# Optimization experiments

Hardware: AMD Instinct MI355X
Metric: run time of the kernel (lower is better)

The kernel has to match this reference:

```python
import jax, jax.numpy as jnp
import numpy as np

B, R, H, IN, L = 8, 128, 256, 512, 3
NH, DH = 4, H // 4  # attention heads


def _layernorm(x, g, b, eps=1e-5):
    mu = jnp.mean(x, axis=-1, keepdims=True)
    var = jnp.mean(jnp.square(x - mu), axis=-1, keepdims=True)
    return (x - mu) * jax.lax.rsqrt(var + eps) * g + b


def setup_inputs() -> dict:
    key = jax.random.key(0)
    ks = iter(jax.random.split(key, 40))
    s = 0.02
    d = {}
    d['x'] = jax.random.normal(next(ks), (B, IN), jnp.float32)
    d['We'] = jax.random.normal(next(ks), (IN, H), jnp.float32) * s
    d['be'] = jnp.zeros((H,), jnp.float32)
    # per-graph-layer params, stacked along leading L axis
    d['msg_W1'] = jax.random.normal(next(ks), (L, 2 * H, H), jnp.float32) * s
    d['msg_b1'] = jnp.zeros((L, H), jnp.float32)
    d['msg_W2'] = jax.random.normal(next(ks), (L, H, H), jnp.float32) * s
    d['msg_b2'] = jnp.zeros((L, H), jnp.float32)
    d['upd_W1'] = jax.random.normal(next(ks), (L, 2 * H, H), jnp.float32) * s
    d['upd_b1'] = jnp.zeros((L, H), jnp.float32)
    d['upd_W2'] = jax.random.normal(next(ks), (L, H, H), jnp.float32) * s
    d['upd_b2'] = jnp.zeros((L, H), jnp.float32)
    d['ln_g'] = jnp.ones((L, H), jnp.float32)
    d['ln_b'] = jnp.zeros((L, H), jnp.float32)
    d['rule_adj'] = jax.random.normal(next(ks), (R, R), jnp.float32)
    # multihead attention (4 heads)
    d['Wq'] = jax.random.normal(next(ks), (H, H), jnp.float32) * s
    d['bq'] = jnp.zeros((H,), jnp.float32)
    d['Wk'] = jax.random.normal(next(ks), (H, H), jnp.float32) * s
    d['bk'] = jnp.zeros((H,), jnp.float32)
    d['Wv'] = jax.random.normal(next(ks), (H, H), jnp.float32) * s
    d['bv'] = jnp.zeros((H,), jnp.float32)
    d['Wo'] = jax.random.normal(next(ks), (H, H), jnp.float32) * s
    d['bo'] = jnp.zeros((H,), jnp.float32)
    # readout MLP -> num_rules logits
    d['ro_W1'] = jax.random.normal(next(ks), (H, H), jnp.float32) * s
    d['ro_b1'] = jnp.zeros((H,), jnp.float32)
    d['ro_W2'] = jax.random.normal(next(ks), (H, R), jnp.float32) * s
    d['ro_b2'] = jnp.zeros((R,), jnp.float32)
    return d


def reference(x, We, be, msg_W1, msg_b1, msg_W2, msg_b2,
              upd_W1, upd_b1, upd_W2, upd_b2, ln_g, ln_b, rule_adj,
              Wq, bq, Wk, bk, Wv, bv, Wo, bo,
              ro_W1, ro_b1, ro_W2, ro_b2):
    # node encoder, broadcast to all rule-graph nodes: [B,R,H]
    h0 = x @ We + be
    h = jnp.broadcast_to(h0[:, None, :], (B, R, H))
    # rule adjacency with self-edges excluded (loop used i != j)
    A = jax.nn.sigmoid(rule_adj) * (1.0 - jnp.eye(R, dtype=rule_adj.dtype))  # [R,R]
    for l in range(L):
        # message_net(cat(h_i, h_j)) = relu(h_i@W1a + h_j@W1b + b1)@W2 + b2
        W1a, W1b = msg_W1[l][:H], msg_W1[l][H:]
        a = h @ W1a   # [B,R,H] (receiver i part)
        bb = h @ W1b  # [B,R,H] (sender j part)
        pre = jax.nn.relu(a[:, :, None, :] + bb[:, None, :, :] + msg_b1[l])  # [B,R,R,H]
        m = pre @ msg_W2[l] + msg_b2[l]  # [B,R,R,H] message from j to i
        agg = jnp.einsum('bijh,ij->bih', m, A)  # weighted sum over senders j
        # update_net(cat(h, agg))
        Wu1a, Wu1b = upd_W1[l][:H], upd_W1[l][H:]
        u = jax.nn.relu(h @ Wu1a + agg @ Wu1b + upd_b1[l]) @ upd_W2[l] + upd_b2[l]
        h = _layernorm(h + u, ln_g[l], ln_b[l])
    # multihead self-attention over nodes
    q = (h @ Wq + bq).reshape(B, R, NH, DH)
    k = (h @ Wk + bk).reshape(B, R, NH, DH)
    v = (h @ Wv + bv).reshape(B, R, NH, DH)
    logits = jnp.einsum('bqhd,bkhd->bhqk', q, k) / jnp.sqrt(jnp.float32(DH))
    attn = jax.nn.softmax(logits, axis=-1)
    pooled = jnp.einsum('bhqk,bkhd->bqhd', attn, v).reshape(B, R, H) @ Wo + bo
    g = jnp.mean(pooled, axis=1)  # [B,H]
    rule_logits = jax.nn.relu(g @ ro_W1 + ro_b1) @ ro_W2 + ro_b2
    rule_probabilities = jax.nn.softmax(rule_logits, axis=-1)  # [B,R]
    return rule_probabilities
```

## Files before the change

kernel.cpp:

```cpp
#include <hip/hip_runtime.h>
#include <math.h>

constexpr int NB  = 8;
constexpr int NR  = 128;
constexpr int HID = 256;
constexpr int NIN = 512;
constexpr int DHD = 64;
constexpr size_t SZ = (size_t)NB * NR * HID;

struct KP {
    const float *x, *We, *be, *msg_W1, *msg_b1, *msg_W2, *msg_b2;
    const float *upd_W1, *upd_b1, *upd_W2, *upd_b2, *ln_g, *ln_b, *rule_adj;
    const float *Wq, *bq, *Wk, *bk, *Wv, *bv, *Wo, *bo, *ro_W1, *ro_b1, *ro_W2, *ro_b2;
    float* out;
    float *N0, *N1, *N2;
    float *aB, *bbB, *p1B;
    float *aA, *bbA, *p1A;
    float *W2u, *mb2u, *Aw, *rsum;
    float *mW1s;
    float *h0g;
    float *c0g, *c1g;
    float *gacc;
    float *scratch;
};

__device__ __forceinline__ void gemm_core(
    float (&As)[16][68], float (&Bs)[16][64], int m0, int n0,
    const float* __restrict__ A, const float* __restrict__ B,
    float (&acc)[4][4])
{
    int tid = threadIdx.x;
    int ty = tid >> 4, tx = tid & 15;
    int arow = tid >> 2, acol = (tid & 3) << 2;
    int brow = tid >> 4, bcol = (tid & 15) << 2;
    int m = m0 + arow;

    float4 av = *(const float4*)&A[(size_t)m * HID + acol];
    float4 bv = *(const float4*)&B[(size_t)brow * HID + n0 + bcol];

    for (int k0 = 0; k0 < HID; k0 += 16) {
        As[acol + 0][arow] = av.x;
        As[acol + 1][arow] = av.y;
        As[acol + 2][arow] = av.z;
        As[acol + 3][arow] = av.w;
        *(float4*)&Bs[brow][bcol] = bv;
        __syncthreads();
        if (k0 + 16 < HID) {
            av = *(const float4*)&A[(size_t)m * HID + k0 + 16 + acol];
            bv = *(const float4*)&B[(size_t)(k0 + 16 + brow) * HID + n0 + bcol];
        }
#pragma unroll
        for (int kk = 0; kk < 16; ++kk) {
            float4 af = *(const float4*)&As[kk][ty << 2];
            float4 bf = *(const float4*)&Bs[kk][tx << 2];
            float a_[4] = {af.x, af.y, af.z, af.w};
            float b_[4] = {bf.x, bf.y, bf.z, bf.w};
#pragma unroll
            for (int i = 0; i < 4; ++i)
#pragma unroll
                for (int j = 0; j < 4; ++j) acc[i][j] += a_[i] * b_[j];
        }
        __syncthreads();
    }
}

__device__ __forceinline__ void gemv256w(
    const float* xs, const float* __restrict__ W,
    const float* __restrict__ bias, int relu, float* ys, float* red)
{
    int tid = threadIdx.x;
    int w = tid >> 6, l = tid & 63;
    float4 acc = {0.f, 0.f, 0.f, 0.f};
    const float* Wp = W + (size_t)(w * 64) * HID + l * 4;
    const float* xp = xs + w * 64;
#pragma unroll 16
    for (int kk = 0; kk < 64; ++kk) {
        float xv = xp[kk];
        float4 wv = *(const float4*)(Wp + (size_t)kk * HID);
        acc.x += xv * wv.x; acc.y += xv * wv.y;
        acc.z += xv * wv.z; acc.w += xv * wv.w;
    }
    *(float4*)&red[w * 256 + l * 4] = acc;
    __syncthreads();
    float v = red[tid] + red[256 + tid] + red[512 + tid] + red[768 + tid];
    if (bias) v += bias[tid];
    if (relu) v = fmaxf(v, 0.0f);
    ys[tid] = v;
    __syncthreads();
}

__device__ __forceinline__ void rows4_q(
    const float (&rows)[4][HID], const float* __restrict__ W,
    int col, int q, float o[4])
{
    o[0] = o[1] = o[2] = o[3] = 0.f;
    int kb = q * 64;
#pragma unroll 4
    for (int k0 = 0; k0 < 64; k0 += 4) {
        int k = kb + k0;
        float w0 = W[(size_t)(k + 0) * HID + col];
        float w1 = W[(size_t)(k + 1) * HID + col];
        float w2 = W[(size_t)(k + 2) * HID + col];
        float w3 = W[(size_t)(k + 3) * HID + col];
#pragma unroll
        for (int ii = 0; ii < 4; ++ii) {
            float4 rv = *(const float4*)&rows[ii][k];
            o[ii] += rv.x * w0 + rv.y * w1 + rv.z * w2 + rv.w * w3;
        }
    }
}

__device__ __forceinline__ void ln_stats4_q(
    float (&sred)[4][4][2], float (&mi)[4][2], const float v[4], int q)
{
    if (q == 0) {
        int w = threadIdx.x >> 6, l = threadIdx.x & 63;
        float s[4], qq[4];
#pragma unroll
        for (int ii = 0; ii < 4; ++ii) { s[ii] = v[ii]; qq[ii] = v[ii] * v[ii]; }
#pragma unroll
        for (int off = 32; off; off >>= 1) {
#pragma unroll
            for (int ii = 0; ii < 4; ++ii) {
                s[ii] += __shfl_xor(s[ii], off);
                qq[ii] += __shfl_xor(qq[ii], off);
            }
        }
        if (l == 0) {
#pragma unroll
            for (int ii = 0; ii < 4; ++ii) { sred[w][ii][0] = s[ii]; sred[w][ii][1] = qq[ii]; }
        }
    }
    __syncthreads();
    if (threadIdx.x < 4) {
        int r = threadIdx.x;
        float ss = sred[0][r][0] + sred[1][r][0] + sred[2][r][0] + sred[3][r][0];
        float qq = sred[0][r][1] + sred[1][r][1] + sred[2][r][1] + sred[3][r][1];
        float mu = ss * (1.0f / HID);
        mi[r][0] = mu;
        mi[r][1] = rsqrtf(qq * (1.0f / HID) - mu * mu + 1e-5f);
    }
    __syncthreads();
}

__global__ __launch_bounds__(256) void setup0_kernel(KP P) {
    __shared__ union {
        struct { float As[16][68]; float Bs[16][64]; } g;
        struct { float xs[NIN]; float part[8][32]; } e;
    } L;
    int blk = blockIdx.x;
    int t = threadIdx.x;

    if (blk < 32) {
        int rr = blk * 4 + (t >> 6);
        int l = t & 63;
        float s_loc = 0.f;
#pragma unroll
        for (int rep = 0; rep < 2; ++rep) {
            int j = l + rep * 64;
            float xv = P.rule_adj[rr * NR + j];
            float sg = 1.0f / (1.0f + expf(-xv));
            if (j == rr) sg = 0.0f;
            P.Aw[rr * NR + j] = sg;
            s_loc += sg;
        }
#pragma unroll
        for (int off = 32; off; off >>= 1) s_loc += __shfl_xor(s_loc, off);
        if (l == 0) P.rsum[rr] = s_loc;
    } else if (blk < 80) {
        int idx = blk - 32, l2 = idx >> 4, t16 = idx & 15;
        int m0 = (t16 >> 2) * 64, n0 = (t16 & 3) * 64;
        float acc[4][4] = {};
        gemm_core(L.g.As, L.g.Bs, m0, n0,
                  P.msg_W2 + (size_t)l2 * HID * HID,
                  P.upd_W1 + (size_t)l2 * 2 * HID * HID + (size_t)HID * HID,
                  acc);
        int ty = t >> 4, tx = t & 15;
        float* C = P.W2u + (size_t)l2 * HID * HID;
#pragma unroll
        for (int i = 0; i < 4; ++i) {
            int m = m0 + (ty << 2) + i, n = n0 + (tx << 2);
            float4 o = {acc[i][0], acc[i][1], acc[i][2], acc[i][3]};
            *(float4*)&C[(size_t)m * HID + n] = o;
        }
    } else if (blk < 83) {
        int l2 = blk - 80;
        const float* b2v = P.msg_b2 + l2 * HID;
        const float* Bm = P.upd_W1 + (size_t)l2 * 2 * HID * HID + (size_t)HID * HID;
        float acc = 0.f;
#pragma unroll 4
        for (int k = 0; k < HID; ++k) acc += b2v[k] * Bm[(size_t)k * HID + t];
        P.mb2u[l2 * HID + t] = acc;
    } else if (blk < 147) {
        int idx = blk - 83;
        int b = idx >> 3, s = idx & 7;
        L.e.xs[t]       = P.x[b * NIN + t];
        L.e.xs[256 + t] = P.x[b * NIN + 256 + t];
        __syncthreads();
        int c = t & 31, seg = t >> 5;
        int col = s * 32 + c;
        const float* Wp = P.We + (size_t)(seg * 64) * HID + col;
        const float* xp = L.e.xs + seg * 64;
        float acc = 0.f;
#pragma unroll 16
        for (int k = 0; k < 64; ++k) acc += xp[k] * Wp[(size_t)k * HID];
        L.e.part[seg][c] = acc;
        __syncthreads();
        if (t < 32) {
            float v = 0.f;
#pragma unroll
            for (int sg = 0; sg < 8; ++sg) v += L.e.part[sg][t];
            int cc = s * 32 + t;
            P.h0g[b * HID + cc] = v + P.be[cc];
        }
    } else if (blk < 163) {
        int base = (blk - 147) * 4096;
        for (int i = t; i < 4096; i += 256) {
            int o = base + i;
            P.mW1s[o] = P.msg_W1[o] + P.msg_W1[65536 + o];
        }
    } else {
        int pfid = blk - 163, npf = 256 - 163;
        const float* arr[11] = {P.We, P.msg_W1, P.msg_W2, P.upd_W1, P.upd_W2,
                                P.Wq, P.Wk, P.Wv, P.Wo, P.ro_W1, P.ro_W2};
        const int n4[11] = {32768, 98304, 49152, 98304, 49152,
                            16384, 16384, 16384, 16384, 16384, 8192};
        float s = 0.f;
        for (int a = 0; a < 11; ++a) {
            const float4* p4 = (const float4*)arr[a];
            for (int i = pfid * 256 + t; i < n4[a]; i += npf * 256) {
                float4 v = p4[i];
                s += v.x + v.y + v.z + v.w;
            }
        }
        if (s == 1.0e37f) P.scratch[pfid] = s;
    }
}

__global__ __launch_bounds__(256) void setup1_kernel(KP P) {
    __shared__ float h0s[HID], c0s[HID], p0s[HID], c1s[HID];
    __shared__ float red[1024];
    int b = blockIdx.x;
    int t = threadIdx.x;
    h0s[t] = P.h0g[b * HID + t];
    __syncthreads();
    gemv256w(h0s, P.upd_W1, nullptr, 0, c0s, red);
    gemv256w(h0s, P.mW1s, P.msg_b1, 1, p0s, red);
    gemv256w(p0s, P.W2u, P.mb2u, 0, c1s, red);
    P.c0g[b * HID + t] = c0s[t];
    P.c1g[b * HID + t] = c1s[t];
}

__global__ __launch_bounds__(1024) void layer0p_kernel(KP P) {
    __shared__ float h0s[HID];
    __shared__ float u1s[4][HID];
    __shared__ float nrm[4][HID];
    __shared__ float part4[4][4][HID];
    __shared__ float sred[4][4][2];
    __shared__ float mi[4][2];
    int blk = blockIdx.x;
    int m0 = blk * 4;
    int b = m0 >> 7, i0 = m0 & 127;
    int t = threadIdx.x;
    int col = t & 255, q = t >> 8;

    if (q == 0) {
        float h0v = P.h0g[b * HID + col];
        h0s[col] = h0v;
        float c0 = P.c0g[b * HID + col];
        float c1 = P.c1g[b * HID + col];
        float ubv = P.upd_b1[col];
#pragma unroll
        for (int ii = 0; ii < 4; ++ii)
            u1s[ii][col] = fmaxf(c0 + P.rsum[i0 + ii] * c1 + ubv, 0.0f);
    }
    __syncthreads();

    float o[4];
    rows4_q(u1s, P.upd_W2, col, q, o);
#pragma unroll
    for (int ii = 0; ii < 4; ++ii) part4[q][ii][col] = o[ii];
    __syncthreads();
    float v[4] = {0.f, 0.f, 0.f, 0.f};
    if (q == 0) {
        float h0v = h0s[col] + P.upd_b2[col];
#pragma unroll
        for (int ii = 0; ii < 4; ++ii)
            v[ii] = part4[0][ii][col] + part4[1][ii][col] + part4[2][ii][col]
                  + part4[3][ii][col] + h0v;
    }
    ln_stats4_q(sred, mi, v, q);
    if (q == 0) {
        float gv = P.ln_g[col], btv = P.ln_b[col];
#pragma unroll
        for (int ii = 0; ii < 4; ++ii) {
            float nv = (v[ii] - mi[ii][0]) * mi[ii][1] * gv + btv;
            nrm[ii][col] = nv;
            P.N0[(size_t)(m0 + ii) * HID + col] = nv;
        }
    }
    __syncthreads();

    const float* mW1a1 = P.msg_W1 + (size_t)1 * 2 * HID * HID;
    const float* uW1a1 = P.upd_W1 + (size_t)1 * 2 * HID * HID;
    const float* pw[3] = {mW1a1, mW1a1 + (size_t)HID * HID, uW1a1};
    float* po[3] = {P.aB, P.bbB, P.p1B};
#pragma unroll
    for (int p = 0; p < 3; ++p) {
        rows4_q(nrm, pw[p], col, q, o);
#pragma unroll
        for (int ii = 0; ii < 4; ++ii) part4[q][ii][col] = o[ii];
        __syncthreads();
        if (q == 0) {
#pragma unroll
            for (int ii = 0; ii < 4; ++ii)
                po[p][(size_t)(m0 + ii) * HID + col] =
                    part4[0][ii][col] + part4[1][ii][col] +
                    part4[2][ii][col] + part4[3][ii][col];
        }
        __syncthreads();
    }
}

__global__ __launch_bounds__(1024) void aggproj_kernel(
    const float* __restrict__ a, const float* __restrict__ bbv,
    const float* __restrict__ mb1, const float* __restrict__ Aw,
    const float* __restrict__ rsumv,
    const float* __restrict__ P1, const float* __restrict__ W2u,
    const float* __restrict__ mb2u, const float* __restrict__ ub1,
    const float* __restrict__ uW2, const float* __restrict__ ub2,
    const float* __restrict__ Nprev, const float* __restrict__ lng,
    const float* __restrict__ lnb, float* __restrict__ Nout,
    const float* __restrict__ pw0, const float* __restrict__ pb0, float* __restrict__ o0,
    const float* __restrict__ pw1, const float* __restrict__ pb1, float* __restrict__ o1,
    const float* __restrict__ pw2, const float* __restrict__ pb2, float* __restrict__ o2,
    float* __restrict__ gzero)
{
    __shared__ float ap[4][HID];
    __shared__ float u1s[4][HID];
    __shared__ float nrm[4][HID];
    __shared__ float awr[4][NR];
    __shared__ float part4[4][4][HID];
    __shared__ float sred[4][4][2];
    __shared__ float mi[4][2];
    int blk = blockIdx.x;
    int b  = blk >> 5;
    int i0 = (blk & 31) * 4;
    int m0 = b * NR + i0;
    int t  = threadIdx.x;
    int col = t & 255, q = t >> 8;

    if (gzero && blk == 0 && q == 0) {
#pragma unroll
        for (int i = 0; i < 8; ++i) gzero[i * 256 + col] = 0.f;
    }

    if (t < 512) awr[t >> 7][t & 127] = Aw[(i0 + (t >> 7)) * NR + (t & 127)];

    float bias = mb1[col];
    float ai[4];
#pragma unroll
    for (int ii = 0; ii < 4; ++ii)
        ai[ii] = a[(size_t)(m0 + ii) * HID + col] + bias;
    __syncthreads();

    {
        float acc[4] = {0.f, 0.f, 0.f, 0.f};
        const float* bbb = &bbv[(size_t)b * NR * HID + col];
        int jb = q * 32;
#pragma unroll 4
        for (int j = 0; j < 32; ++j) {
            float bj = bbb[(size_t)(jb + j) * HID];
#pragma unroll
            for (int ii = 0; ii < 4; ++ii) {
                float pre = fmaxf(ai[ii] + bj, 0.0f);
                acc[ii] += awr[ii][jb + j] * pre;
            }
        }
#pragma unroll
        for (int ii = 0; ii < 4; ++ii) part4[q][ii][col] = acc[ii];
        __syncthreads();
        if (q == 0) {
#pragma unroll
            for (int ii = 0; ii < 4; ++ii)
                ap[ii][col] = part4[0][ii][col] + part4[1][ii][col]
                            + part4[2][ii][col] + part4[3][ii][col];
        }
        __syncthreads();
    }

    {
        float o[4];
        rows4_q(ap, W2u, col, q, o);
#pragma unroll
        for (int ii = 0; ii < 4; ++ii) part4[q][ii][col] = o[ii];
        __syncthreads();
        if (q == 0) {
            float mbv = mb2u[col], ubv = ub1[col];
#pragma unroll
            for (int ii = 0; ii < 4; ++ii) {
                float w2f = part4[0][ii][col] + part4[1][ii][col]
                          + part4[2][ii][col] + part4[3][ii][col];
                float vv = w2f + P1[(size_t)(m0 + ii) * HID + col]
                         + rsumv[i0 + ii] * mbv + ubv;
                u1s[ii][col] = fmaxf(vv, 0.0f);
            }
        }
        __syncthreads();
    }

    {
        float o[4];
        rows4_q(u1s, uW2, col, q, o);
#pragma unroll
        for (int ii = 0; ii < 4; ++ii) part4[q][ii][col] = o[ii];
        __syncthreads();
        float v[4] = {0.f, 0.f, 0.f, 0.f};
        if (q == 0) {
            float ub2v = ub2[col];
#pragma unroll
            for (int ii = 0; ii < 4; ++ii) {
                float uf = part4[0][ii][col] + part4[1][ii][col]
                         + part4[2][ii][col] + part4[3][ii][col];
                v[ii] = Nprev[(size_t)(m0 + ii) * HID + col] + uf + ub2v;
            }
        }
        ln_stats4_q(sred, mi, v, q);
        if (q == 0) {
            float gv = lng[col], btv = lnb[col];
#pragma unroll
            for (int ii = 0; ii < 4; ++ii) {
                float nv = (v[ii] - mi[ii][0]) * mi[ii][1] * gv + btv;
                nrm[ii][col] = nv;
                Nout[(size_t)(m0 + ii) * HID + col] = nv;
            }
        }
        __syncthreads();
    }

    {
        const float* pw[3] = {pw0, pw1, pw2};
        const float* pb[3] = {pb0, pb1, pb2};
        float* po[3] = {o0, o1, o2};
#pragma unroll
        for (int p = 0; p < 3; ++p) {
            float o[4];
            rows4_q(nrm, pw[p], col, q, o);
#pragma unroll
            for (int ii = 0; ii < 4; ++ii) part4[q][ii][col] = o[ii];
            __syncthreads();
            if (q == 0) {
                float pbv = pb[p] ? pb[p][col] : 0.f;
#pragma unroll
                for (int ii = 0; ii < 4; ++ii)
                    po[p][(size_t)(m0 + ii) * HID + col] =
                        part4[0][ii][col] + part4[1][ii][col] +
                        part4[2][ii][col] + part4[3][ii][col] + pbv;
            }
            __syncthreads();
        }
    }
}

__global__ __launch_bounds__(256) void attention_kernel(
    const float* __restrict__ q, const float* __restrict__ k,
    const float* __restrict__ v, float* __restrict__ gacc)
{
    __shared__ struct { float KhT[64][128]; float S[16][128]; float qs[16][64]; } L;
    int blk = blockIdx.x;
    int bh = blk >> 3, ig = blk & 7;
    int b = bh >> 2, hd = bh & 3;
    int i0 = ig * 16;
    int t = threadIdx.x;
    const float* qg = q + ((size_t)b * NR) * HID + hd * DHD;
    const float* kg = k + ((size_t)b * NR) * HID + hd * DHD;
    const float* vg = v + ((size_t)b * NR) * HID + hd * DHD;

    {
        int j = t >> 1, half = t & 1;
        const float* krow = kg + (size_t)j * HID + half * 32;
#pragma unroll
        for (int c = 0; c < 32; c += 4) {
            float4 kv = *(const float4*)(krow + c);
            L.KhT[half * 32 + c + 0][j] = kv.x;
            L.KhT[half * 32 + c + 1][j] = kv.y;
            L.KhT[half * 32 + c + 2][j] = kv.z;
            L.KhT[half * 32 + c + 3][j] = kv.w;
        }
    }
    {
        int ii = t >> 4, d0 = (t & 15) * 4;
        *(float4*)&L.qs[ii][d0] = *(const float4*)(qg + (size_t)(i0 + ii) * HID + d0);
    }
    __syncthreads();
    {
        int j = t & 127, ii2 = t >> 7;
        float acc[8] = {0.f,0.f,0.f,0.f,0.f,0.f,0.f,0.f};
#pragma unroll 4
        for (int d = 0; d < 64; ++d) {
            float kv = L.KhT[d][j];
#pragma unroll
            for (int ii = 0; ii < 8; ++ii) acc[ii] += L.qs[ii2 * 8 + ii][d] * kv;
        }
#pragma unroll
        for (int ii = 0; ii < 8; ++ii) L.S[ii2 * 8 + ii][j] = acc[ii] * 0.125f;
    }
    __syncthreads();
    {
        int w = t >> 6, l = t & 63;
#pragma unroll
        for (int r = w * 4; r < w * 4 + 4; ++r) {
            float e0 = L.S[r][l], e1 = L.S[r][l + 64];
            float mx = fmaxf(e0, e1);
#pragma unroll
            for (int off = 32; off; off >>= 1) mx = fmaxf(mx, __shfl_xor(mx, off));
            e0 = expf(e0 - mx); e1 = expf(e1 - mx);
            float sm = e0 + e1;
#pragma unroll
            for (int off = 32; off; off >>= 1) sm += __shfl_xor(sm, off);
            float inv = 1.0f / sm;
            L.S[r][l] = e0 * inv; L.S[r][l + 64] = e1 * inv;
        }
    }
    __syncthreads();
    {
        int d = t & 63, ir = t >> 6;
        float accv[4] = {0.f, 0.f, 0.f, 0.f};
        const float* vp = vg + d;
#pragma unroll 8
        for (int j = 0; j < NR; ++j) {
            float vv = vp[(size_t)j * HID];
#pragma unroll
            for (int p = 0; p < 4; ++p) accv[p] += L.S[p * 4 + ir][j] * vv;
        }
        float s = accv[0] + accv[1] + accv[2] + accv[3];
        atomicAdd(&gacc[b * HID + hd * DHD + d], s);
    }
}

__global__ __launch_bounds__(256) void tailf_kernel(KP P) {
    __shared__ float v0[HID], v1[HID], v2[HID];
    __shared__ float red[1024];
    int b = blockIdx.x;
    int t = threadIdx.x;
    int w = t >> 6, l = t & 63;

    v0[t] = P.gacc[b * HID + t] * (1.0f / NR);
    __syncthreads();
    gemv256w(v0, P.Wo, P.bo, 0, v1, red);
    gemv256w(v1, P.ro_W1, P.ro_b1, 1, v2, red);

    {
        float2 acc = {0.f, 0.f};
        const float* Wp = P.ro_W2 + (size_t)(w * 64) * NR + l * 2;
        const float* xp = v2 + w * 64;
#pragma unroll 8
        for (int kk = 0; kk < 64; ++kk) {
            float xv = xp[kk];
            float2 wv = *(const float2*)(Wp + (size_t)kk * NR);
            acc.x += xv * wv.x; acc.y += xv * wv.y;
        }
        *(float2*)&red[w * 128 + l * 2] = acc;
        __syncthreads();
    }
    float logit = -1e30f;
    if (t < NR) logit = red[t] + red[128 + t] + red[256 + t] + red[384 + t] + P.ro_b2[t];
    __syncthreads();
    float m = logit;
#pragma unroll
    for (int off = 32; off; off >>= 1) m = fmaxf(m, __shfl_xor(m, off));
    if (l == 0) red[w] = m;
    __syncthreads();
    m = fmaxf(red[0], red[1]);
    float e = (t < NR) ? expf(logit - m) : 0.0f;
    float ssum = e;
#pragma unroll
    for (int off = 32; off; off >>= 1) ssum += __shfl_xor(ssum, off);
    if (l == 0) red[4 + w] = ssum;
    __syncthreads();
    float tot = red[4] + red[5];
    if (t < NR) P.out[b * NR + t] = e / tot;
}

extern "C" void kernel_launch(void* const* d_in, const int* in_sizes, int n_in,
                              void* d_out, int out_size, void* d_ws, size_t ws_size,
                              hipStream_t stream)
{
    KP P;
    P.x        = (const float*)d_in[0];
    P.We       = (const float*)d_in[1];
    P.be       = (const float*)d_in[2];
    P.msg_W1   = (const float*)d_in[3];
    P.msg_b1   = (const float*)d_in[4];
    P.msg_W2   = (const float*)d_in[5];
    P.msg_b2   = (const float*)d_in[6];
    P.upd_W1   = (const float*)d_in[7];
    P.upd_b1   = (const float*)d_in[8];
    P.upd_W2   = (const float*)d_in[9];
    P.upd_b2   = (const float*)d_in[10];
    P.ln_g     = (const float*)d_in[11];
    P.ln_b     = (const float*)d_in[12];
    P.rule_adj = (const float*)d_in[13];
    P.Wq       = (const float*)d_in[14];
    P.bq       = (const float*)d_in[15];
    P.Wk       = (const float*)d_in[16];
    P.bk       = (const float*)d_in[17];
    P.Wv       = (const float*)d_in[18];
    P.bv       = (const float*)d_in[19];
    P.Wo       = (const float*)d_in[20];
    P.bo       = (const float*)d_in[21];
    P.ro_W1    = (const float*)d_in[22];
    P.ro_b1    = (const float*)d_in[23];
    P.ro_W2    = (const float*)d_in[24];
    P.ro_b2    = (const float*)d_in[25];
    P.out      = (float*)d_out;

    float* b0 = (float*)d_ws;
    P.N0     = b0;  b0 += SZ;
    P.N1     = b0;  b0 += SZ;
    P.N2     = b0;  b0 += SZ;
    P.aB     = b0;  b0 += SZ;
    P.bbB    = b0;  b0 += SZ;
    P.p1B    = b0;  b0 += SZ;
    P.aA     = b0;  b0 += SZ;
    P.bbA    = b0;  b0 += SZ;
    P.p1A    = b0;  b0 += SZ;
    P.W2u    = b0;  b0 += 3 * HID * HID;
    P.mb2u   = b0;  b0 += 3 * HID;
    P.mW1s   = b0;  b0 += HID * HID;
    P.Aw     = b0;  b0 += NR * NR;
    P.rsum   = b0;  b0 += NR;
    P.h0g    = b0;  b0 += NB * HID;
    P.c0g    = b0;  b0 += NB * HID;
    P.c1g    = b0;  b0 += NB * HID;
    P.gacc   = b0;  b0 += NB * HID;
    P.scratch= b0;  b0 += 256;

    setup0_kernel<<<dim3(256), 256, 0, stream>>>(P);

    setup1_kernel<<<dim3(8), 256, 0, stream>>>(P);

    layer0p_kernel<<<dim3(256), 1024, 0, stream>>>(P);

    {
        const int l = 1;
        const float* mW1a2 = P.msg_W1 + (size_t)2 * 2 * HID * HID;
        const float* uW1a2 = P.upd_W1 + (size_t)2 * 2 * HID * HID;
        aggproj_kernel<<<dim3(256), 1024, 0, stream>>>(
            P.aB, P.bbB, P.msg_b1 + (size_t)l * HID, P.Aw, P.rsum,
            P.p1B, P.W2u + (size_t)l * HID * HID, P.mb2u + l * HID,
            P.upd_b1 + (size_t)l * HID,
            P.upd_W2 + (size_t)l * HID * HID, P.upd_b2 + (size_t)l * HID,
            P.N0, P.ln_g + (size_t)l * HID, P.ln_b + (size_t)l * HID, P.N1,
            mW1a2, nullptr, P.aA,
            mW1a2 + (size_t)HID * HID, nullptr, P.bbA,
            uW1a2, nullptr, P.p1A,
            nullptr);
    }

    {
        const int l = 2;
        aggproj_kernel<<<dim3(256), 1024, 0, stream>>>(
            P.aA, P.bbA, P.msg_b1 + (size_t)l * HID, P.Aw, P.rsum,
            P.p1A, P.W2u + (size_t)l * HID * HID, P.mb2u + l * HID,
            P.upd_b1 + (size_t)l * HID,
            P.upd_W2 + (size_t)l * HID * HID, P.upd_b2 + (size_t)l * HID,
            P.N1, P.ln_g + (size_t)l * HID, P.ln_b + (size_t)l * HID, P.N2,
            P.Wq, P.bq, P.aB,
            P.Wk, P.bk, P.bbB,
            P.Wv, P.bv, P.p1B,
            P.gacc);
    }

    attention_kernel<<<dim3(256), 256, 0, stream>>>(P.aB, P.bbB, P.p1B, P.gacc);

    tailf_kernel<<<dim3(8), 256, 0, stream>>>(P);
}
```

Baseline: 231.0 us.

## Spread reductions across all warp groups and fuse three projection GEMVs

```diff
diff --git a/kernel.cpp b/kernel.cpp
--- a/kernel.cpp
+++ b/kernel.cpp
@@ -110,37 +110,37 @@
     }
 }
 
-__device__ __forceinline__ void ln_stats4_q(
-    float (&sred)[4][4][2], float (&mi)[4][2], const float v[4], int q)
+__device__ __forceinline__ void rows4_q3(
+    const float (&rows)[4][HID],
+    const float* __restrict__ W0, const float* __restrict__ W1,
+    const float* __restrict__ W2m,
+    int col, int q, float o[3][4])
 {
-    if (q == 0) {
-        int w = threadIdx.x >> 6, l = threadIdx.x & 63;
-        float s[4], qq[4];
-#pragma unroll
-        for (int ii = 0; ii < 4; ++ii) { s[ii] = v[ii]; qq[ii] = v[ii] * v[ii]; }
-#pragma unroll
-        for (int off = 32; off; off >>= 1) {
-#pragma unroll
-            for (int ii = 0; ii < 4; ++ii) {
-                s[ii] += __shfl_xor(s[ii], off);
-                qq[ii] += __shfl_xor(qq[ii], off);
-            }
-        }
-        if (l == 0) {
-#pragma unroll
-            for (int ii = 0; ii < 4; ++ii) { sred[w][ii][0] = s[ii]; sred[w][ii][1] = qq[ii]; }
-        }
-    }
-    __syncthreads();
-    if (threadIdx.x < 4) {
-        int r = threadIdx.x;
-        float ss = sred[0][r][0] + sred[1][r][0] + sred[2][r][0] + sred[3][r][0];
-        float qq = sred[0][r][1] + sred[1][r][1] + sred[2][r][1] + sred[3][r][1];
-        float mu = ss * (1.0f / HID);
-        mi[r][0] = mu;
-        mi[r][1] = rsqrtf(qq * (1.0f / HID) - mu * mu + 1e-5f);
-    }
-    __syncthreads();
+#pragma unroll
+    for (int p = 0; p < 3; ++p)
+#pragma unroll
+        for (int ii = 0; ii < 4; ++ii) o[p][ii] = 0.f;
+    int kb = q * 64;
+#pragma unroll 2
+    for (int k0 = 0; k0 < 64; k0 += 4) {
+        int k = kb + k0;
+        float4 rv[4];
+#pragma unroll
+        for (int ii = 0; ii < 4; ++ii) rv[ii] = *(const float4*)&rows[ii][k];
+        const float* Wp[3] = {W0, W1, W2m};
+#pragma unroll
+        for (int p = 0; p < 3; ++p) {
+            const float* W = Wp[p];
+            float w0 = W[(size_t)(k + 0) * HID + col];
+            float w1 = W[(size_t)(k + 1) * HID + col];
+            float w2 = W[(size_t)(k + 2) * HID + col];
+            float w3 = W[(size_t)(k + 3) * HID + col];
+#pragma unroll
+            for (int ii = 0; ii < 4; ++ii)
+                o[p][ii] += rv[ii].x * w0 + rv[ii].y * w1
+                          + rv[ii].z * w2 + rv[ii].w * w3;
+        }
+    }
 }
 
 __global__ __launch_bounds__(256) void setup0_kernel(KP P) {
@@ -255,70 +255,75 @@
     __shared__ float h0s[HID];
     __shared__ float u1s[4][HID];
     __shared__ float nrm[4][HID];
-    __shared__ float part4[4][4][HID];
+    __shared__ float part3[3][4][4][HID];
     __shared__ float sred[4][4][2];
-    __shared__ float mi[4][2];
     int blk = blockIdx.x;
     int m0 = blk * 4;
     int b = m0 >> 7, i0 = m0 & 127;
     int t = threadIdx.x;
     int col = t & 255, q = t >> 8;
-
-    if (q == 0) {
-        float h0v = P.h0g[b * HID + col];
-        h0s[col] = h0v;
+    int w4 = (t >> 6) & 3, l = t & 63;
+
+    {
         float c0 = P.c0g[b * HID + col];
         float c1 = P.c1g[b * HID + col];
+        if (q == 0) h0s[col] = P.h0g[b * HID + col];
         float ubv = P.upd_b1[col];
-#pragma unroll
-        for (int ii = 0; ii < 4; ++ii)
-            u1s[ii][col] = fmaxf(c0 + P.rsum[i0 + ii] * c1 + ubv, 0.0f);
-    }
-    __syncthreads();
-
-    float o[4];
-    rows4_q(u1s, P.upd_W2, col, q, o);
-#pragma unroll
-    for (int ii = 0; ii < 4; ++ii) part4[q][ii][col] = o[ii];
-    __syncthreads();
-    float v[4] = {0.f, 0.f, 0.f, 0.f};
-    if (q == 0) {
+        u1s[q][col] = fmaxf(c0 + P.rsum[i0 + q] * c1 + ubv, 0.0f);
+    }
+    __syncthreads();
+
+    {
+        float o[4];
+        rows4_q(u1s, P.upd_W2, col, q, o);
+#pragma unroll
+        for (int ii = 0; ii < 4; ++ii) part3[0][q][ii][col] = o[ii];
+    }
+    __syncthreads();
+
+    float v;
+    {
         float h0v = h0s[col] + P.upd_b2[col];
-#pragma unroll
-        for (int ii = 0; ii < 4; ++ii)
-            v[ii] = part4[0][ii][col] + part4[1][ii][col] + part4[2][ii][col]
-                  + part4[3][ii][col] + h0v;
-    }
-    ln_stats4_q(sred, mi, v, q);
-    if (q == 0) {
-        float gv = P.ln_g[col], btv = P.ln_b[col];
+        v = part3[0][0][q][col] + part3[0][1][q][col]
+          + part3[0][2][q][col] + part3[0][3][q][col] + h0v;
+        float s = v, qq2 = v * v;
+#pragma unroll
+        for (int off = 32; off; off >>= 1) {
+            s += __shfl_xor(s, off); qq2 += __shfl_xor(qq2, off);
+        }
+        if (l == 0) { sred[q][w4][0] = s; sred[q][w4][1] = qq2; }
+    }
+    __syncthreads();
+    {
+        float ss  = sred[q][0][0] + sred[q][1][0] + sred[q][2][0] + sred[q][3][0];
+        float qq2 = sred[q][0][1] + sred[q][1][1] + sred[q][2][1] + sred[q][3][1];
+        float mu = ss * (1.0f / HID);
+        float inv = rsqrtf(qq2 * (1.0f / HID) - mu * mu + 1e-5f);
+        float nv = (v - mu) * inv * P.ln_g[col] + P.ln_b[col];
+        nrm[q][col] = nv;
+        P.N0[(size_t)(m0 + q) * HID + col] = nv;
+    }
+    __syncthreads();
+
+    {
+        const float* mW1a1 = P.msg_W1 + (size_t)1 * 2 * HID * HID;
+        const float* uW1a1 = P.upd_W1 + (size_t)1 * 2 * HID * HID;
+        float o3[3][4];
+        rows4_q3(nrm, mW1a1, mW1a1 + (size_t)HID * HID, uW1a1, col, q, o3);
+#pragma unroll
+        for (int p = 0; p < 3; ++p)
+#pragma unroll
+            for (int ii = 0; ii < 4; ++ii) part3[p][q][ii][col] = o3[p][ii];
+    }
+    __syncthreads();
+    if (q < 3) {
+        float* po = (q == 0) ? P.aB : (q == 1) ? P.bbB : P.p1B;
 #pragma unroll
         for (int ii = 0; ii < 4; ++ii) {
-            float nv = (v[ii] - mi[ii][0]) * mi[ii][1] * gv + btv;
-            nrm[ii][col] = nv;
-            P.N0[(size_t)(m0 + ii) * HID + col] = nv;
-        }
-    }
-    __syncthreads();
-
-    const float* mW1a1 = P.msg_W1 + (size_t)1 * 2 * HID * HID;
-    const float* uW1a1 = P.upd_W1 + (size_t)1 * 2 * HID * HID;
-    const float* pw[3] = {mW1a1, mW1a1 + (size_t)HID * HID, uW1a1};
-    float* po[3] = {P.aB, P.bbB, P.p1B};
-#pragma unroll
-    for (int p = 0; p < 3; ++p) {
-        rows4_q(nrm, pw[p], col, q, o);
-#pragma unroll
-        for (int ii = 0; ii < 4; ++ii) part4[q][ii][col] = o[ii];
-        __syncthreads();
-        if (q == 0) {
-#pragma unroll
-            for (int ii = 0; ii < 4; ++ii)
-                po[p][(size_t)(m0 + ii) * HID + col] =
-                    part4[0][ii][col] + part4[1][ii][col] +
-                    part4[2][ii][col] + part4[3][ii][col];
-        }
-        __syncthreads();
+            float s = part3[q][0][ii][col] + part3[q][1][ii][col]
+                    + part3[q][2][ii][col] + part3[q][3][ii][col];
+            po[(size_t)(m0 + ii) * HID + col] = s;
+        }
     }
 }
 
@@ -340,15 +345,15 @@
     __shared__ float u1s[4][HID];
     __shared__ float nrm[4][HID];
     __shared__ float awr[4][NR];
-    __shared__ float part4[4][4][HID];
+    __shared__ float part3[3][4][4][HID];
     __shared__ float sred[4][4][2];
-    __shared__ float mi[4][2];
     int blk = blockIdx.x;
     int b  = blk >> 5;
     int i0 = (blk & 31) * 4;
     int m0 = b * NR + i0;
     int t  = threadIdx.x;
     int col = t & 255, q = t >> 8;
+    int w4 = (t >> 6) & 3, l = t & 63;
 
     if (gzero && blk == 0 && q == 0) {
 #pragma unroll
@@ -378,86 +383,78 @@
             }
         }
 #pragma unroll
-        for (int ii = 0; ii < 4; ++ii) part4[q][ii][col] = acc[ii];
-        __syncthreads();
-        if (q == 0) {
-#pragma unroll
-            for (int ii = 0; ii < 4; ++ii)
-                ap[ii][col] = part4[0][ii][col] + part4[1][ii][col]
-                            + part4[2][ii][col] + part4[3][ii][col];
-        }
-        __syncthreads();
-    }
+        for (int ii = 0; ii < 4; ++ii) part3[0][q][ii][col] = acc[ii];
+    }
+    __syncthreads();
+    ap[q][col] = part3[0][0][q][col] + part3[0][1][q][col]
+               + part3[0][2][q][col] + part3[0][3][q][col];
+    __syncthreads();
 
     {
         float o[4];
         rows4_q(ap, W2u, col, q, o);
 #pragma unroll
-        for (int ii = 0; ii < 4; ++ii) part4[q][ii][col] = o[ii];
-        __syncthreads();
-        if (q == 0) {
-            float mbv = mb2u[col], ubv = ub1[col];
-#pragma unroll
-            for (int ii = 0; ii < 4; ++ii) {
-                float w2f = part4[0][ii][col] + part4[1][ii][col]
-                          + part4[2][ii][col] + part4[3][ii][col];
-                float vv = w2f + P1[(size_t)(m0 + ii) * HID + col]
-                         + rsumv[i0 + ii] * mbv + ubv;
-                u1s[ii][col] = fmaxf(vv, 0.0f);
-            }
-        }
-        __syncthreads();
-    }
+        for (int ii = 0; ii < 4; ++ii) part3[0][q][ii][col] = o[ii];
+    }
+    __syncthreads();
+    {
+        float w2f = part3[0][0][q][col] + part3[0][1][q][col]
+                  + part3[0][2][q][col] + part3[0][3][q][col];
+        float vv = w2f + P1[(size_t)(m0 + q) * HID + col]
+                 + rsumv[i0 + q] * mb2u[col] + ub1[col];
+        u1s[q][col] = fmaxf(vv, 0.0f);
+    }
+    __syncthreads();
 
     {
         float o[4];
         rows4_q(u1s, uW2, col, q, o);
 #pragma unroll
-        for (int ii = 0; ii < 4; ++ii) part4[q][ii][col] = o[ii];
-        __syncthreads();
-        float v[4] = {0.f, 0.f, 0.f, 0.f};
-        if (q == 0) {
-            float ub2v = ub2[col];
-#pragma unroll
-            for (int ii = 0; ii < 4; ++ii) {
-                float uf = part4[0][ii][col] + part4[1][ii][col]
-                         + part4[2][ii][col] + part4[3][ii][col];
-                v[ii] = Nprev[(size_t)(m0 + ii) * HID + col] + uf + ub2v;
-            }
-        }
-        ln_stats4_q(sred, mi, v, q);
-        if (q == 0) {
-            float gv = lng[col], btv = lnb[col];
-#pragma unroll
-            for (int ii = 0; ii < 4; ++ii) {
-                float nv = (v[ii] - mi[ii][0]) * mi[ii][1] * gv + btv;
-                nrm[ii][col] = nv;
-                Nout[(size_t)(m0 + ii) * HID + col] = nv;
-            }
-        }
-        __syncthreads();
-    }
-
-    {
-        const float* pw[3] = {pw0, pw1, pw2};
-        const float* pb[3] = {pb0, pb1, pb2};
-        float* po[3] = {o0, o1, o2};
-#pragma unroll
-        for (int p = 0; p < 3; ++p) {
-            float o[4];
-            rows4_q(nrm, pw[p], col, q, o);
-#pragma unroll
-            for (int ii = 0; ii < 4; ++ii) part4[q][ii][col] = o[ii];
-            __syncthreads();
-            if (q == 0) {
-                float pbv = pb[p] ? pb[p][col] : 0.f;
-#pragma unroll
-                for (int ii = 0; ii < 4; ++ii)
-                    po[p][(size_t)(m0 + ii) * HID + col] =
-                        part4[0][ii][col] + part4[1][ii][col] +
-                        part4[2][ii][col] + part4[3][ii][col] + pbv;
-            }
-            __syncthreads();
+        for (int ii = 0; ii < 4; ++ii) part3[0][q][ii][col] = o[ii];
+    }
+    __syncthreads();
+    float v;
+    {
+        float uf = part3[0][0][q][col] + part3[0][1][q][col]
+                 + part3[0][2][q][col] + part3[0][3][q][col];
+        v = Nprev[(size_t)(m0 + q) * HID + col] + uf + ub2[col];
+        float s = v, qq2 = v * v;
+#pragma unroll
+        for (int off = 32; off; off >>= 1) {
+            s += __shfl_xor(s, off); qq2 += __shfl_xor(qq2, off);
+        }
+        if (l == 0) { sred[q][w4][0] = s; sred[q][w4][1] = qq2; }
+    }
+    __syncthreads();
+    {
+        float ss  = sred[q][0][0] + sred[q][1][0] + sred[q][2][0] + sred[q][3][0];
+        float qq2 = sred[q][0][1] + sred[q][1][1] + sred[q][2][1] + sred[q][3][1];
+        float mu = ss * (1.0f / HID);
+        float inv = rsqrtf(qq2 * (1.0f / HID) - mu * mu + 1e-5f);
+        float nv = (v - mu) * inv * lng[col] + lnb[col];
+        nrm[q][col] = nv;
+        Nout[(size_t)(m0 + q) * HID + col] = nv;
+    }
+    __syncthreads();
+
+    {
+        float o3[3][4];
+        rows4_q3(nrm, pw0, pw1, pw2, col, q, o3);
+#pragma unroll
+        for (int p = 0; p < 3; ++p)
+#pragma unroll
+            for (int ii = 0; ii < 4; ++ii) part3[p][q][ii][col] = o3[p][ii];
+    }
+    __syncthreads();
+    if (q < 3) {
+        const float* pb = (q == 0) ? pb0 : (q == 1) ? pb1 : pb2;
+        float* po = (q == 0) ? o0 : (q == 1) ? o1 : o2;
+        float pbv = pb ? pb[col] : 0.f;
+#pragma unroll
+        for (int ii = 0; ii < 4; ++ii) {
+            float s = part3[q][0][ii][col] + part3[q][1][ii][col]
+                    + part3[q][2][ii][col] + part3[q][3][ii][col] + pbv;
+            po[(size_t)(m0 + ii) * HID + col] = s;
         }
     }
 }
```

Measured after the change: 224.5 us. 2.8% less time.
